# Optimization experiments

Hardware: AMD Instinct MI355X
Metric: run time of the kernel (lower is better)

## Reference

```python
import jax, jax.numpy as jnp
import numpy as np
from jax import lax

B, T, D, H, O, L = 128, 2048, 64, 128, 32, 2


def _rnn_layer(x, lengths, W_ih, W_hh, b_ih, b_hh):
    """One tanh RNN layer over padded [B,T,*] input with packed semantics:
    hidden state is frozen at steps t >= lengths[b] (those steps do not exist
    in the packed sequence). Returns per-step hidden states [B,T,H]."""
    Bl, Tl, _ = x.shape
    Hl = W_hh.shape[0]
    # precompute input projection once: [B,T,H]
    x_proj = jnp.einsum('btd,hd->bth', x, W_ih) + b_ih + b_hh

    def step(h, inp):
        xp, t = inp  # xp: [B,H], t: scalar
        h_new = jnp.tanh(xp + h @ W_hh.T)
        h = jnp.where((t < lengths)[:, None], h_new, h)
        return h, h

    h0 = jnp.zeros((Bl, Hl), dtype=x.dtype)
    _, ys = lax.scan(step, h0, (x_proj.transpose(1, 0, 2), jnp.arange(Tl)))
    return ys.transpose(1, 0, 2)  # [B,T,H]


def setup_inputs() -> dict:
    key = jax.random.key(0)
    ks = jax.random.split(key, 12)
    x = jax.random.normal(ks[0], (B, T, D), dtype=jnp.float32)
    # descending-sorted lengths in [1, T] (pack_padded_sequence enforce_sorted)
    lengths = jnp.sort(jax.random.randint(ks[1], (B,), 1, T + 1).astype(jnp.int32))[::-1]
    s_in = 1.0 / np.sqrt(H)
    W_ih0 = jax.random.uniform(ks[2], (H, D), minval=-s_in, maxval=s_in)
    W_hh0 = jax.random.uniform(ks[3], (H, H), minval=-s_in, maxval=s_in)
    b_ih0 = jax.random.uniform(ks[4], (H,), minval=-s_in, maxval=s_in)
    b_hh0 = jax.random.uniform(ks[5], (H,), minval=-s_in, maxval=s_in)
    W_ih1 = jax.random.uniform(ks[6], (H, H), minval=-s_in, maxval=s_in)
    W_hh1 = jax.random.uniform(ks[7], (H, H), minval=-s_in, maxval=s_in)
    b_ih1 = jax.random.uniform(ks[8], (H,), minval=-s_in, maxval=s_in)
    b_hh1 = jax.random.uniform(ks[9], (H,), minval=-s_in, maxval=s_in)
    W_fc = jax.random.uniform(ks[10], (O, H), minval=-s_in, maxval=s_in)
    b_fc = jax.random.uniform(ks[11], (O,), minval=-s_in, maxval=s_in)
    return {"x": x, "lengths": lengths,
            "W_ih0": W_ih0, "W_hh0": W_hh0, "b_ih0": b_ih0, "b_hh0": b_hh0,
            "W_ih1": W_ih1, "W_hh1": W_hh1, "b_ih1": b_ih1, "b_hh1": b_hh1,
            "W_fc": W_fc, "b_fc": b_fc}


def reference(x, lengths, W_ih0, W_hh0, b_ih0, b_hh0,
              W_ih1, W_hh1, b_ih1, b_hh1, W_fc, b_fc):
    h1 = _rnn_layer(x, lengths, W_ih0, W_hh0, b_ih0, b_hh0)   # [B,T,H]
    h2 = _rnn_layer(h1, lengths, W_ih1, W_hh1, b_ih1, b_hh1)  # [B,T,H]
    # pad_packed_sequence zero-fills positions t >= length
    mask = (jnp.arange(T)[None, :] < lengths[:, None])[..., None]
    out = jnp.where(mask, h2, 0.0)
    # fc is applied to the zero-padded tensor (padded rows become b_fc)
    return jnp.einsum('bth,oh->bto', out, W_fc) + b_fc
```

## Files before the change

### kernel.cpp

```cpp
#include <hip/hip_runtime.h>

#define BB 128
#define TT 2048
#define DD 64
#define HH 128
#define OO 32
#define NB 16
#define SCALE 2.885390081777927f

typedef _Float16 f16x8 __attribute__((ext_vector_type(8)));
typedef __fp16   pk16x2 __attribute__((ext_vector_type(2)));
typedef float    f32x4 __attribute__((ext_vector_type(4)));

#define MFMA16(a,b,c) __builtin_amdgcn_mfma_f32_16x16x32_f16((a),(b),(c),0,0,0)

__device__ __forceinline__ f32x4 load4(const float* p){ return *(const f32x4*)p; }

__device__ __forceinline__ f16x8 afrag_s(const float* p, float s){
    float4 a = *(const float4*)p, b = *(const float4*)(p+4);
    f16x8 r;
    r[0]=(_Float16)(a.x*s); r[1]=(_Float16)(a.y*s); r[2]=(_Float16)(a.z*s); r[3]=(_Float16)(a.w*s);
    r[4]=(_Float16)(b.x*s); r[5]=(_Float16)(b.y*s); r[6]=(_Float16)(b.z*s); r[7]=(_Float16)(b.w*s);
    return r;
}

__device__ __forceinline__ float tanh_pre(float z){
#if __has_builtin(__builtin_amdgcn_exp2f)
    float e = __builtin_amdgcn_exp2f(z);
#else
    float e = exp2f(z);
#endif
    return __builtin_fmaf(-2.f, __builtin_amdgcn_rcpf(1.f + e), 1.f);
}

__device__ __forceinline__ unsigned pk2(float a, float b){
    union { pk16x2 h; unsigned u; } c;
    c.h = __builtin_amdgcn_cvt_pkrtz(a, b);
    return c.u;
}

#define XSTR 72
extern "C" __global__ void __launch_bounds__(256)
proj_kernel(const float* __restrict__ x, const float* __restrict__ W_ih0,
            const float* __restrict__ b_ih0, const float* __restrict__ b_hh0,
            _Float16* __restrict__ xp0)
{
    const int tid = threadIdx.x;
    const int w = tid >> 6, lane = tid & 63;
    const int n = lane & 15, q = lane >> 4;
    const size_t row0 = (size_t)blockIdx.x * 64;

    __shared__ __align__(16) _Float16 XT[64][XSTR];

    #pragma unroll
    for (int it = 0; it < 4; ++it){
        float4 v = *(const float4*)(x + row0*DD + it*1024 + tid*4);
        int rr = it*16 + (tid >> 4), d0 = (tid & 15)*4;
        union { uint2 u; _Float16 h[4]; } c;
        c.h[0]=(_Float16)v.x; c.h[1]=(_Float16)v.y; c.h[2]=(_Float16)v.z; c.h[3]=(_Float16)v.w;
        *(uint2*)&XT[rr][d0] = c.u;
    }

    f16x8 A[8][2]; f32x4 bv[8];
    #pragma unroll
    for (int mt = 0; mt < 8; ++mt){
        #pragma unroll
        for (int kt = 0; kt < 2; ++kt)
            A[mt][kt] = afrag_s(W_ih0 + (mt*16 + n)*DD + kt*32 + q*8, SCALE);
        bv[mt] = (load4(b_ih0 + mt*16 + q*4) + load4(b_hh0 + mt*16 + q*4)) * SCALE;
    }
    __syncthreads();

    const _Float16* xr = &XT[w*16 + n][0];
    f16x8 B0 = *(const f16x8*)(xr + q*8);
    f16x8 B1 = *(const f16x8*)(xr + 32 + q*8);

    _Float16* orow = xp0 + (row0 + w*16 + n)*HH + q*4;
    #pragma unroll
    for (int mt = 0; mt < 8; ++mt){
        f32x4 acc = bv[mt];
        acc = MFMA16(A[mt][0], B0, acc);
        acc = MFMA16(A[mt][1], B1, acc);
        union { uint2 u; _Float16 h[4]; } s;
        #pragma unroll
        for (int r = 0; r < 4; ++r) s.h[r] = (_Float16)acc[r];
        *(uint2*)(orow + mt*16) = s.u;
    }
}

extern "C" __global__ void __launch_bounds__(256)
fill_kernel(const int* __restrict__ lengths, const float* __restrict__ b_fc,
            float* __restrict__ out)
{
    size_t idx = (size_t)blockIdx.x*256 + threadIdx.x;
    #pragma unroll
    for (int k = 0; k < 4; ++k, idx += (size_t)2048*256){
        int o4 = (int)(idx & 7);
        int t  = (int)((idx >> 3) & 2047);
        int b  = (int)(idx >> 14);
        if (t >= lengths[b])
            ((float4*)out)[idx] = *(const float4*)(b_fc + o4*4);
    }
}

#define LSTR 136

#define STEP(T_, P_, XA_, XB_) do {                                           \
    const int t_ = (T_);                                                      \
    f16x8 bh1[4], bh2[4];                                                     \
    _Pragma("unroll")                                                         \
    for (int kt = 0; kt < 4; ++kt){                                           \
        bh1[kt] = *(const f16x8*)&H1T[P_][n][kt*32 + q*8];                    \
        bh2[kt] = *(const f16x8*)&H2T[P_][n][kt*32 + q*8];                    \
    }                                                                         \
    f32x4 z0[2];                                                              \
    const bool doZ0 = (t_ < maxlen);                                          \
    if (doZ0){                                                                \
        union { uint2 u; _Float16 h[4]; } cA, cB; cA.u = XA_; cB.u = XB_;     \
        _Pragma("unroll")                                                     \
        for (int r = 0; r < 4; ++r){ z0[0][r] = (float)cA.h[r];               \
                                     z0[1][r] = (float)cB.h[r]; }             \
        _Pragma("unroll")                                                     \
        for (int kt = 0; kt < 4; ++kt){                                       \
            z0[0] = MFMA16(A0[0][kt], bh1[kt], z0[0]);                        \
            z0[1] = MFMA16(A0[1][kt], bh1[kt], z0[1]);                        \
        }                                                                     \
    }                                                                         \
    {              \
        const int tl = (t_ + 2 < TT) ? (t_ + 2) : (TT - 1);                   \
        XA_ = *(const uint2*)(xpbase + (size_t)tl*HH);                        \
        XB_ = *(const uint2*)(xpbase + (size_t)tl*HH + 16);                   \
    }                                                                         \
    f32x4 z1[2];                                                              \
    const bool doZ1 = (t_ >= 1) && (t_ <= maxlen);                            \
    if (doZ1){                                                                \
        f32x4 y0, y1;                                                         \
        z1[0] = b1v[0]; z1[1] = b1v[1];                                       \
        y0[0]=0.f;y0[1]=0.f;y0[2]=0.f;y0[3]=0.f; y1=y0;                       \
        _Pragma("unroll")                                                     \
        for (int kt = 0; kt < 4; ++kt){                                       \
            z1[0] = MFMA16(Ai[0][kt], bh1[kt], z1[0]);                        \
            z1[1] = MFMA16(Ai[1][kt], bh1[kt], z1[1]);                        \
            y0    = MFMA16(Ah[0][kt], bh2[kt], y0);                           \
            y1    = MFMA16(Ah[1][kt], bh2[kt], y1);                           \
        }                                                                     \
        z1[0] += y0; z1[1] += y1;                                             \
    }                                                                         \
    if (w >= 2 && t_ >= 2){                                                   \
        f32x4 zf = bfv;                                                       \
        _Pragma("unroll")                                                     \
        for (int kt = 0; kt < 4; ++kt) zf = MFMA16(Af[kt], bh2[kt], zf);      \
        if (t_ - 2 < lenn){                                                   \
            float4 sv; sv.x=zf[0]; sv.y=zf[1]; sv.z=zf[2]; sv.w=zf[3];        \
            *(float4*)(obase + (size_t)(t_-2)*OO) = sv;                       \
        }                                                                     \
    }                                                                         \
    if (doZ0){                                                                \
        _Pragma("unroll")                                                     \
        for (int m = 0; m < 2; ++m){                                          \
            uint2 v;                                                          \
            v.x = pk2(tanh_pre(z0[m][0]), tanh_pre(z0[m][1]));                \
            v.y = pk2(tanh_pre(z0[m][2]), tanh_pre(z0[m][3]));                \
            *(uint2*)&H1T[(P_)^1][n][(2*w+m)*16 + q*4] = v;                   \
        }                                                                     \
    }                                                                         \
    if (doZ1){                                                                \
        _Pragma("unroll")                                                     \
        for (int m = 0; m < 2; ++m){                                          \
            uint2 v;                                                          \
            v.x = pk2(tanh_pre(z1[m][0]), tanh_pre(z1[m][1]));                \
            v.y = pk2(tanh_pre(z1[m][2]), tanh_pre(z1[m][3]));                \
            *(uint2*)&H2T[(P_)^1][n][(2*w+m)*16 + q*4] = v;                   \
        }                                                                     \
    }                                                                         \
    asm volatile("s_waitcnt lgkmcnt(0)\n\ts_barrier" ::: "memory");           \
} while (0)

extern "C" __global__ void __launch_bounds__(256, 1)
scan_kernel(const _Float16* __restrict__ xp0, const int* __restrict__ lengths,
            const float* __restrict__ W_hh0,
            const float* __restrict__ W_ih1, const float* __restrict__ W_hh1,
            const float* __restrict__ b_ih1, const float* __restrict__ b_hh1,
            const float* __restrict__ W_fc,  const float* __restrict__ b_fc,
            float* __restrict__ out)
{
    const int tid  = threadIdx.x;
    const int w    = tid >> 6, lane = tid & 63;
    const int n    = lane & 15, q = lane >> 4;
    const int rbase= blockIdx.x * NB;

    __shared__ __align__(16) _Float16 H1T[2][NB][LSTR];
    __shared__ __align__(16) _Float16 H2T[2][NB][LSTR];

    for (int idx = tid; idx < 2*NB*LSTR/2; idx += 256){
        ((unsigned*)H1T)[idx] = 0u;
        ((unsigned*)H2T)[idx] = 0u;
    }

    f16x8 A0[2][4], Ai[2][4], Ah[2][4];
    #pragma unroll
    for (int m = 0; m < 2; ++m){
        const int row = (2*w + m)*16 + n;
        #pragma unroll
        for (int kt = 0; kt < 4; ++kt){
            A0[m][kt] = afrag_s(W_hh0 + row*HH + kt*32 + q*8, SCALE);
            Ai[m][kt] = afrag_s(W_ih1 + row*HH + kt*32 + q*8, SCALE);
            Ah[m][kt] = afrag_s(W_hh1 + row*HH + kt*32 + q*8, SCALE);
        }
    }
    const int f = w & 1;
    f16x8 Af[4];
    #pragma unroll
    for (int kt = 0; kt < 4; ++kt)
        Af[kt] = afrag_s(W_fc + (f*16 + n)*HH + kt*32 + q*8, 1.0f);

    f32x4 b1v[2];
    #pragma unroll
    for (int m = 0; m < 2; ++m)
        b1v[m] = (load4(b_ih1 + (2*w+m)*16 + q*4) + load4(b_hh1 + (2*w+m)*16 + q*4)) * SCALE;
    const f32x4 bfv = load4(b_fc + f*16 + q*4);

    const int lenn = lengths[rbase + n];
    int mx = lenn;
    #pragma unroll
    for (int s = 1; s < 16; s <<= 1){ int o = __shfl_xor(mx, s, 64); mx = max(mx, o); }
    const int maxlen = __builtin_amdgcn_readfirstlane(mx);

    const _Float16* xpbase = xp0 + ((size_t)(rbase+n)*TT)*HH + (2*w)*16 + q*4;
    float* obase = out + ((size_t)(rbase+n)*TT)*OO + f*16 + q*4;

    uint2 xeA = *(const uint2*)(xpbase);
    uint2 xeB = *(const uint2*)(xpbase + 16);
    uint2 xoA = *(const uint2*)(xpbase + HH);
    uint2 xoB = *(const uint2*)(xpbase + HH + 16);

    __syncthreads();

    for (int t0 = 0; t0 <= maxlen + 1; t0 += 2){
        STEP(t0,     0, xeA, xeB);
        STEP(t0 + 1, 1, xoA, xoB);
    }
}

extern "C" void kernel_launch(void* const* d_in, const int* in_sizes, int n_in,
                              void* d_out, int out_size, void* d_ws, size_t ws_size,
                              hipStream_t stream)
{
    const float* x       = (const float*)d_in[0];
    const int*   lengths = (const int*)  d_in[1];
    const float* W_ih0   = (const float*)d_in[2];
    const float* W_hh0   = (const float*)d_in[3];
    const float* b_ih0   = (const float*)d_in[4];
    const float* b_hh0   = (const float*)d_in[5];
    const float* W_ih1   = (const float*)d_in[6];
    const float* W_hh1   = (const float*)d_in[7];
    const float* b_ih1   = (const float*)d_in[8];
    const float* b_hh1   = (const float*)d_in[9];
    const float* W_fc    = (const float*)d_in[10];
    const float* b_fc    = (const float*)d_in[11];

    _Float16* xp = (_Float16*)d_ws;

    proj_kernel<<<BB*TT/64, 256, 0, stream>>>(x, W_ih0, b_ih0, b_hh0, xp);
    fill_kernel<<<2048, 256, 0, stream>>>(lengths, b_fc, (float*)d_out);
    scan_kernel<<<BB/NB, 256, 0, stream>>>(xp, lengths, W_hh0,
                                           W_ih1, W_hh1, b_ih1, b_hh1,
                                           W_fc, b_fc, (float*)d_out);
}
```

Before: 1.637 ms.

## Specialize warps: two run layer-1 recurrence, two run layer-2 plus FC

Splits the four wavefronts by role: waves 0-1 compute the layer-1 recurrence over all 128 hidden rows (4 row-tiles each), and waves 2-3 compute the layer-2 recurrence plus the output projection. Before, every wave did a slice of both layers. The LDS row stride changes from 136 to 132 halves, and B fragments are loaded as two 8-byte reads to suit the new stride. The aim is to balance MFMA work per wave and cut the per-wave register load of weight fragments. In exchange, layer 1 now does fewer MFMAs per step than layer 2, so the waves may be imbalanced at the shared barrier, and register pressure per wave rises.

Result: no change. 1.631 ms (-0.3%).

```diff
diff --git a/kernel.cpp b/kernel.cpp
--- a/kernel.cpp
+++ b/kernel.cpp
@@ -15,6 +15,8 @@
 #define MFMA16(a,b,c) __builtin_amdgcn_mfma_f32_16x16x32_f16((a),(b),(c),0,0,0)
 
 __device__ __forceinline__ f32x4 load4(const float* p){ return *(const f32x4*)p; }
+
+union U8 { uint2 u[2]; f16x8 v; };
 
 __device__ __forceinline__ f16x8 afrag_s(const float* p, float s){
     float4 a = *(const float4*)p, b = *(const float4*)(p+4);
@@ -103,74 +105,95 @@
     }
 }
 
-#define LSTR 136
-
-#define STEP(T_, P_, XA_, XB_) do {                                           \
+#define LSTR2 132
+#define PHB   (NB*LSTR2*2)
+
+#define STEP_L1(T_, P_, XS_) do {                                             \
     const int t_ = (T_);                                                      \
-    f16x8 bh1[4], bh2[4];                                                     \
+    U8 bh1[4];                                                                \
     _Pragma("unroll")                                                         \
     for (int kt = 0; kt < 4; ++kt){                                           \
-        bh1[kt] = *(const f16x8*)&H1T[P_][n][kt*32 + q*8];                    \
-        bh2[kt] = *(const f16x8*)&H2T[P_][n][kt*32 + q*8];                    \
-    }                                                                         \
-    f32x4 z0[2];                                                              \
+        bh1[kt].u[0] = *(const uint2*)(h1b + (P_)*PHB + kt*64);               \
+        bh1[kt].u[1] = *(const uint2*)(h1b + (P_)*PHB + kt*64 + 8);           \
+    }                                                                         \
+    f32x4 z[4];                                                               \
     const bool doZ0 = (t_ < maxlen);                                          \
     if (doZ0){                                                                \
-        union { uint2 u; _Float16 h[4]; } cA, cB; cA.u = XA_; cB.u = XB_;     \
-        _Pragma("unroll")                                                     \
-        for (int r = 0; r < 4; ++r){ z0[0][r] = (float)cA.h[r];               \
-                                     z0[1][r] = (float)cB.h[r]; }             \
-        _Pragma("unroll")                                                     \
-        for (int kt = 0; kt < 4; ++kt){                                       \
-            z0[0] = MFMA16(A0[0][kt], bh1[kt], z0[0]);                        \
-            z0[1] = MFMA16(A0[1][kt], bh1[kt], z0[1]);                        \
-        }                                                                     \
-    }                                                                         \
-    {              \
+        _Pragma("unroll")                                                     \
+        for (int m = 0; m < 4; ++m){                                          \
+            union { uint2 u; _Float16 h[4]; } c; c.u = XS_[m];                \
+            _Pragma("unroll")                                                 \
+            for (int r = 0; r < 4; ++r) z[m][r] = (float)c.h[r];              \
+        }                                                                     \
+        _Pragma("unroll")                                                     \
+        for (int kt = 0; kt < 4; ++kt)                                        \
+            _Pragma("unroll")                                                 \
+            for (int m = 0; m < 4; ++m)                                       \
+                z[m] = MFMA16(A0[m][kt], bh1[kt].v, z[m]);                    \
+    }                                                                         \
+    {             \
         const int tl = (t_ + 2 < TT) ? (t_ + 2) : (TT - 1);                   \
-        XA_ = *(const uint2*)(xpbase + (size_t)tl*HH);                        \
-        XB_ = *(const uint2*)(xpbase + (size_t)tl*HH + 16);                   \
-    }                                                                         \
-    f32x4 z1[2];                                                              \
+        _Pragma("unroll")                                                     \
+        for (int m = 0; m < 4; ++m)                                           \
+            XS_[m] = *(const uint2*)(xpb + (size_t)tl*256 + m*32);            \
+    }                                                                         \
+    if (doZ0){                                                                \
+        _Pragma("unroll")                                                     \
+        for (int m = 0; m < 4; ++m){                                          \
+            uint2 v;                                                          \
+            v.x = pk2(tanh_pre(z[m][0]), tanh_pre(z[m][1]));                  \
+            v.y = pk2(tanh_pre(z[m][2]), tanh_pre(z[m][3]));                  \
+            *(uint2*)((char*)H1T + ((P_)^1)*PHB + n*264 + (w*4+m)*32 + q*8) = v; \
+        }                                                                     \
+    }                                                                         \
+    asm volatile("s_waitcnt lgkmcnt(0)\n\ts_barrier" ::: "memory");           \
+} while (0)
+
+#define STEP_L2(T_, P_) do {                                                  \
+    const int t_ = (T_);                                                      \
+    U8 bh1[4], bh2[4];                                                        \
+    _Pragma("unroll")                                                         \
+    for (int kt = 0; kt < 4; ++kt){                                           \
+        bh1[kt].u[0] = *(const uint2*)(h1b + (P_)*PHB + kt*64);               \
+        bh1[kt].u[1] = *(const uint2*)(h1b + (P_)*PHB + kt*64 + 8);           \
+        bh2[kt].u[0] = *(const uint2*)(h2b + (P_)*PHB + kt*64);               \
+        bh2[kt].u[1] = *(const uint2*)(h2b + (P_)*PHB + kt*64 + 8);           \
+    }                                                                         \
     const bool doZ1 = (t_ >= 1) && (t_ <= maxlen);                            \
+    f32x4 z[4];                                                               \
     if (doZ1){                                                                \
-        f32x4 y0, y1;                                                         \
-        z1[0] = b1v[0]; z1[1] = b1v[1];                                       \
-        y0[0]=0.f;y0[1]=0.f;y0[2]=0.f;y0[3]=0.f; y1=y0;                       \
-        _Pragma("unroll")                                                     \
-        for (int kt = 0; kt < 4; ++kt){                                       \
-            z1[0] = MFMA16(Ai[0][kt], bh1[kt], z1[0]);                        \
-            z1[1] = MFMA16(Ai[1][kt], bh1[kt], z1[1]);                        \
-            y0    = MFMA16(Ah[0][kt], bh2[kt], y0);                           \
-            y1    = MFMA16(Ah[1][kt], bh2[kt], y1);                           \
-        }                                                                     \
-        z1[0] += y0; z1[1] += y1;                                             \
-    }                                                                         \
-    if (w >= 2 && t_ >= 2){                                                   \
+        f32x4 y[4];                                                           \
+        _Pragma("unroll")                                                     \
+        for (int m = 0; m < 4; ++m){                                          \
+            z[m] = b1v[m];                                                    \
+            y[m][0]=0.f; y[m][1]=0.f; y[m][2]=0.f; y[m][3]=0.f;               \
+        }                                                                     \
+        _Pragma("unroll")                                                     \
+        for (int kt = 0; kt < 4; ++kt)                                        \
+            _Pragma("unroll")                                                 \
+            for (int m = 0; m < 4; ++m){                                      \
+                z[m] = MFMA16(Ai[m][kt], bh1[kt].v, z[m]);                    \
+                y[m] = MFMA16(Ah[m][kt], bh2[kt].v, y[m]);                    \
+            }                                                                 \
+        _Pragma("unroll")                                                     \
+        for (int m = 0; m < 4; ++m) z[m] += y[m];                             \
+    }                                                                         \
+    if (t_ >= 2){                                                             \
         f32x4 zf = bfv;                                                       \
         _Pragma("unroll")                                                     \
-        for (int kt = 0; kt < 4; ++kt) zf = MFMA16(Af[kt], bh2[kt], zf);      \
+        for (int kt = 0; kt < 4; ++kt) zf = MFMA16(Af[kt], bh2[kt].v, zf);    \
         if (t_ - 2 < lenn){                                                   \
             float4 sv; sv.x=zf[0]; sv.y=zf[1]; sv.z=zf[2]; sv.w=zf[3];        \
             *(float4*)(obase + (size_t)(t_-2)*OO) = sv;                       \
         }                                                                     \
     }                                                                         \
-    if (doZ0){                                                                \
-        _Pragma("unroll")                                                     \
-        for (int m = 0; m < 2; ++m){                                          \
+    if (doZ1){                                                                \
+        _Pragma("unroll")                                                     \
+        for (int m = 0; m < 4; ++m){                                          \
             uint2 v;                                                          \
-            v.x = pk2(tanh_pre(z0[m][0]), tanh_pre(z0[m][1]));                \
-            v.y = pk2(tanh_pre(z0[m][2]), tanh_pre(z0[m][3]));                \
-            *(uint2*)&H1T[(P_)^1][n][(2*w+m)*16 + q*4] = v;                   \
-        }                                                                     \
-    }                                                                         \
-    if (doZ1){                                                                \
-        _Pragma("unroll")                                                     \
-        for (int m = 0; m < 2; ++m){                                          \
-            uint2 v;                                                          \
-            v.x = pk2(tanh_pre(z1[m][0]), tanh_pre(z1[m][1]));                \
-            v.y = pk2(tanh_pre(z1[m][2]), tanh_pre(z1[m][3]));                \
-            *(uint2*)&H2T[(P_)^1][n][(2*w+m)*16 + q*4] = v;                   \
+            v.x = pk2(tanh_pre(z[m][0]), tanh_pre(z[m][1]));                  \
+            v.y = pk2(tanh_pre(z[m][2]), tanh_pre(z[m][3]));                  \
+            *(uint2*)((char*)H2T + ((P_)^1)*PHB + n*264 + (wl*4+m)*32 + q*8) = v; \
         }                                                                     \
     }                                                                         \
     asm volatile("s_waitcnt lgkmcnt(0)\n\ts_barrier" ::: "memory");           \
@@ -189,56 +212,75 @@
     const int n    = lane & 15, q = lane >> 4;
     const int rbase= blockIdx.x * NB;
 
-    __shared__ __align__(16) _Float16 H1T[2][NB][LSTR];
-    __shared__ __align__(16) _Float16 H2T[2][NB][LSTR];
-
-    for (int idx = tid; idx < 2*NB*LSTR/2; idx += 256){
+    __shared__ __align__(16) _Float16 H1T[2][NB][LSTR2];
+    __shared__ __align__(16) _Float16 H2T[2][NB][LSTR2];
+
+    for (int idx = tid; idx < (2*NB*LSTR2)/2; idx += 256){
         ((unsigned*)H1T)[idx] = 0u;
         ((unsigned*)H2T)[idx] = 0u;
     }
 
-    f16x8 A0[2][4], Ai[2][4], Ah[2][4];
-    #pragma unroll
-    for (int m = 0; m < 2; ++m){
-        const int row = (2*w + m)*16 + n;
-        #pragma unroll
-        for (int kt = 0; kt < 4; ++kt){
-            A0[m][kt] = afrag_s(W_hh0 + row*HH + kt*32 + q*8, SCALE);
-            Ai[m][kt] = afrag_s(W_ih1 + row*HH + kt*32 + q*8, SCALE);
-            Ah[m][kt] = afrag_s(W_hh1 + row*HH + kt*32 + q*8, SCALE);
-        }
-    }
-    const int f = w & 1;
-    f16x8 Af[4];
-    #pragma unroll
-    for (int kt = 0; kt < 4; ++kt)
-        Af[kt] = afrag_s(W_fc + (f*16 + n)*HH + kt*32 + q*8, 1.0f);
-
-    f32x4 b1v[2];
-    #pragma unroll
-    for (int m = 0; m < 2; ++m)
-        b1v[m] = (load4(b_ih1 + (2*w+m)*16 + q*4) + load4(b_hh1 + (2*w+m)*16 + q*4)) * SCALE;
-    const f32x4 bfv = load4(b_fc + f*16 + q*4);
-
     const int lenn = lengths[rbase + n];
     int mx = lenn;
     #pragma unroll
     for (int s = 1; s < 16; s <<= 1){ int o = __shfl_xor(mx, s, 64); mx = max(mx, o); }
     const int maxlen = __builtin_amdgcn_readfirstlane(mx);
 
-    const _Float16* xpbase = xp0 + ((size_t)(rbase+n)*TT)*HH + (2*w)*16 + q*4;
-    float* obase = out + ((size_t)(rbase+n)*TT)*OO + f*16 + q*4;
-
-    uint2 xeA = *(const uint2*)(xpbase);
-    uint2 xeB = *(const uint2*)(xpbase + 16);
-    uint2 xoA = *(const uint2*)(xpbase + HH);
-    uint2 xoB = *(const uint2*)(xpbase + HH + 16);
+    const char* h1b = (const char*)H1T + n*264 + q*16;
+    const char* h2b = (const char*)H2T + n*264 + q*16;
 
     __syncthreads();
 
-    for (int t0 = 0; t0 <= maxlen + 1; t0 += 2){
-        STEP(t0,     0, xeA, xeB);
-        STEP(t0 + 1, 1, xoA, xoB);
+    if (w < 2){
+        f16x8 A0[4][4];
+        #pragma unroll
+        for (int m = 0; m < 4; ++m){
+            const int row = (w*4 + m)*16 + n;
+            #pragma unroll
+            for (int kt = 0; kt < 4; ++kt)
+                A0[m][kt] = afrag_s(W_hh0 + row*HH + kt*32 + q*8, SCALE);
+        }
+        const char* xpb = (const char*)(xp0 + ((size_t)(rbase+n)*TT)*HH)
+                          + (w*4)*32 + q*8;
+
+        uint2 xe[4], xo[4];
+        #pragma unroll
+        for (int m = 0; m < 4; ++m){
+            xe[m] = *(const uint2*)(xpb + m*32);
+            xo[m] = *(const uint2*)(xpb + 256 + m*32);
+        }
+
+        for (int t0 = 0; t0 <= maxlen + 1; t0 += 2){
+            STEP_L1(t0,     0, xe);
+            STEP_L1(t0 + 1, 1, xo);
+        }
+    } else {
+        const int wl = w - 2, f = w & 1;
+        f16x8 Ai[4][4], Ah[4][4];
+        f32x4 b1v[4];
+        #pragma unroll
+        for (int m = 0; m < 4; ++m){
+            const int row = (wl*4 + m)*16 + n;
+            #pragma unroll
+            for (int kt = 0; kt < 4; ++kt){
+                Ai[m][kt] = afrag_s(W_ih1 + row*HH + kt*32 + q*8, SCALE);
+                Ah[m][kt] = afrag_s(W_hh1 + row*HH + kt*32 + q*8, SCALE);
+            }
+            b1v[m] = (load4(b_ih1 + (wl*4+m)*16 + q*4)
+                    + load4(b_hh1 + (wl*4+m)*16 + q*4)) * SCALE;
+        }
+        f16x8 Af[4];
+        #pragma unroll
+        for (int kt = 0; kt < 4; ++kt)
+            Af[kt] = afrag_s(W_fc + (f*16 + n)*HH + kt*32 + q*8, 1.0f);
+        const f32x4 bfv = load4(b_fc + f*16 + q*4);
+
+        float* obase = out + ((size_t)(rbase+n)*TT)*OO + f*16 + q*4;
+
+        for (int t0 = 0; t0 <= maxlen + 1; t0 += 2){
+            STEP_L2(t0,     0);
+            STEP_L2(t0 + 1, 1);
+        }
     }
 }
 
```

## Split RNN scan into layer-specialized waves with LDS ring and windowed barriers

Applied to the files above, without the earlier changes.

Replaces the 4-wave scan block, where every wave computed a slice of both layers and synchronized each step, with a 2-wave block. Wave 0 runs layer 0 over all 128 hidden units, and wave 1 runs layer 1 plus the FC projection. Layer-0 states go through an 8-slot LDS ring, with one barrier per 4-step window, so the layers run as a software pipeline offset by one window. Wave 0 reads its own just-written state back from LDS with no barrier, and a XOR swizzle is added for bank conflicts. The trade-off is that each wave does 4x the MFMA work serially per step and occupancy is lower, in exchange for far fewer barriers.

Measured after the change: 2.945 ms. 1.8x slower.

```diff
diff --git a/kernel.cpp b/kernel.cpp
--- a/kernel.cpp
+++ b/kernel.cpp
@@ -103,80 +103,89 @@
     }
 }
 
-#define LSTR 136
-
-#define STEP(T_, P_, XA_, XB_) do {                                           \
+#define SLOT  (NB*256)
+#define RING  8
+#define KWIN  4
+
+#define STEPA(T_, XS_) do {                                                   \
+    const int t_ = (T_);                                                      \
+    f32x4 z[8];                                                               \
+    _Pragma("unroll")                                                         \
+    for (int mt = 0; mt < 8; ++mt){                                           \
+        union { uint2 u; _Float16 h[4]; } c; c.u = XS_[mt];                   \
+        _Pragma("unroll")                                                     \
+        for (int r = 0; r < 4; ++r) z[mt][r] = (float)c.h[r];                 \
+    }                                                                         \
+    _Pragma("unroll")                                                         \
+    for (int kt = 0; kt < 4; ++kt)                                            \
+        _Pragma("unroll")                                                     \
+        for (int mt = 0; mt < 8; ++mt)                                        \
+            z[mt] = MFMA16(A0[mt][kt], Wst[kt], z[mt]);                       \
+    {   const int tl = (t_ + 2 < TT) ? (t_ + 2) : (TT - 1);                   \
+        const char* xq = xpb + (size_t)tl*256;                                \
+        _Pragma("unroll")                                                     \
+        for (int mt = 0; mt < 8; ++mt) XS_[mt] = *(const uint2*)(xq + mt*32); \
+    }                                                                         \
+    {   char* wp = h1p + ((t_ & 7) * SLOT);                                   \
+        _Pragma("unroll")                                                     \
+        for (int mt = 0; mt < 8; ++mt){                                       \
+            uint2 v;                                                          \
+            v.x = pk2(tanh_pre(z[mt][0]), tanh_pre(z[mt][1]));                \
+            v.y = pk2(tanh_pre(z[mt][2]), tanh_pre(z[mt][3]));                \
+            *(uint2*)(wp + woff[mt]) = v;                                     \
+        }                                                                     \
+        _Pragma("unroll")                                                     \
+        for (int kt = 0; kt < 4; ++kt)                                        \
+            Wst[kt] = *(const f16x8*)((const char*)wp + roff[kt]);            \
+    }                                                                         \
+} while (0)
+
+#define STEPB(T_) do {                                                        \
     const int t_ = (T_);                                                      \
     f16x8 bh1[4], bh2[4];                                                     \
-    _Pragma("unroll")                                                         \
-    for (int kt = 0; kt < 4; ++kt){                                           \
-        bh1[kt] = *(const f16x8*)&H1T[P_][n][kt*32 + q*8];                    \
-        bh2[kt] = *(const f16x8*)&H2T[P_][n][kt*32 + q*8];                    \
-    }                                                                         \
-    f32x4 z0[2];                                                              \
-    const bool doZ0 = (t_ < maxlen);                                          \
-    if (doZ0){                                                                \
-        union { uint2 u; _Float16 h[4]; } cA, cB; cA.u = XA_; cB.u = XB_;     \
-        _Pragma("unroll")                                                     \
-        for (int r = 0; r < 4; ++r){ z0[0][r] = (float)cA.h[r];               \
-                                     z0[1][r] = (float)cB.h[r]; }             \
+    {   const char* rp1 = h1p + ((t_ & 7) * SLOT);                            \
+        const char* rp2 = h2p + ((~t_ & 1) * SLOT);                           \
         _Pragma("unroll")                                                     \
         for (int kt = 0; kt < 4; ++kt){                                       \
-            z0[0] = MFMA16(A0[0][kt], bh1[kt], z0[0]);                        \
-            z0[1] = MFMA16(A0[1][kt], bh1[kt], z0[1]);                        \
+            bh1[kt] = *(const f16x8*)(rp1 + roff[kt]);                        \
+            bh2[kt] = *(const f16x8*)(rp2 + roff[kt]);                        \
+        } }                                                                   \
+    f32x4 z[8];                                                               \
+    _Pragma("unroll")                                                         \
+    for (int mt = 0; mt < 8; ++mt) z[mt] = b1v[mt];                           \
+    _Pragma("unroll")                                                         \
+    for (int kt = 0; kt < 4; ++kt)                                            \
+        _Pragma("unroll")                                                     \
+        for (int mt = 0; mt < 8; ++mt)                                        \
+            z[mt] = MFMA16(Ai[mt][kt], bh1[kt], z[mt]);                       \
+    _Pragma("unroll")                                                         \
+    for (int kt = 0; kt < 4; ++kt)                                            \
+        _Pragma("unroll")                                                     \
+        for (int mt = 0; mt < 8; ++mt)                                        \
+            z[mt] = MFMA16(Ah[mt][kt], bh2[kt], z[mt]);                       \
+    {   f32x4 zf0 = bfv0, zf1 = bfv1;                                         \
+        _Pragma("unroll")                                                     \
+        for (int kt = 0; kt < 4; ++kt){                                       \
+            zf0 = MFMA16(Af[0][kt], bh2[kt], zf0);                            \
+            zf1 = MFMA16(Af[1][kt], bh2[kt], zf1);                            \
         }                                                                     \
-    }                                                                         \
-    {              \
-        const int tl = (t_ + 2 < TT) ? (t_ + 2) : (TT - 1);                   \
-        XA_ = *(const uint2*)(xpbase + (size_t)tl*HH);                        \
-        XB_ = *(const uint2*)(xpbase + (size_t)tl*HH + 16);                   \
-    }                                                                         \
-    f32x4 z1[2];                                                              \
-    const bool doZ1 = (t_ >= 1) && (t_ <= maxlen);                            \
-    if (doZ1){                                                                \
-        f32x4 y0, y1;                                                         \
-        z1[0] = b1v[0]; z1[1] = b1v[1];                                       \
-        y0[0]=0.f;y0[1]=0.f;y0[2]=0.f;y0[3]=0.f; y1=y0;                       \
-        _Pragma("unroll")                                                     \
-        for (int kt = 0; kt < 4; ++kt){                                       \
-            z1[0] = MFMA16(Ai[0][kt], bh1[kt], z1[0]);                        \
-            z1[1] = MFMA16(Ai[1][kt], bh1[kt], z1[1]);                        \
-            y0    = MFMA16(Ah[0][kt], bh2[kt], y0);                           \
-            y1    = MFMA16(Ah[1][kt], bh2[kt], y1);                           \
-        }                                                                     \
-        z1[0] += y0; z1[1] += y1;                                             \
-    }                                                                         \
-    if (w >= 2 && t_ >= 2){                                                   \
-        f32x4 zf = bfv;                                                       \
-        _Pragma("unroll")                                                     \
-        for (int kt = 0; kt < 4; ++kt) zf = MFMA16(Af[kt], bh2[kt], zf);      \
-        if (t_ - 2 < lenn){                                                   \
-            float4 sv; sv.x=zf[0]; sv.y=zf[1]; sv.z=zf[2]; sv.w=zf[3];        \
-            *(float4*)(obase + (size_t)(t_-2)*OO) = sv;                       \
-        }                                                                     \
-    }                                                                         \
-    if (doZ0){                                                                \
-        _Pragma("unroll")                                                     \
-        for (int m = 0; m < 2; ++m){                                          \
+        if ((unsigned)(t_ - 1) < (unsigned)lenn){                             \
+            float* op = obase + (size_t)(t_ - 1) * OO;                        \
+            float4 s0; s0.x=zf0[0]; s0.y=zf0[1]; s0.z=zf0[2]; s0.w=zf0[3];    \
+            float4 s1; s1.x=zf1[0]; s1.y=zf1[1]; s1.z=zf1[2]; s1.w=zf1[3];    \
+            *(float4*)op = s0; *(float4*)(op + 16) = s1;                      \
+        } }                                                                   \
+    {   char* wp = h2p + ((t_ & 1) * SLOT);                                   \
+        _Pragma("unroll")                                                     \
+        for (int mt = 0; mt < 8; ++mt){                                       \
             uint2 v;                                                          \
-            v.x = pk2(tanh_pre(z0[m][0]), tanh_pre(z0[m][1]));                \
-            v.y = pk2(tanh_pre(z0[m][2]), tanh_pre(z0[m][3]));                \
-            *(uint2*)&H1T[(P_)^1][n][(2*w+m)*16 + q*4] = v;                   \
-        }                                                                     \
-    }                                                                         \
-    if (doZ1){                                                                \
-        _Pragma("unroll")                                                     \
-        for (int m = 0; m < 2; ++m){                                          \
-            uint2 v;                                                          \
-            v.x = pk2(tanh_pre(z1[m][0]), tanh_pre(z1[m][1]));                \
-            v.y = pk2(tanh_pre(z1[m][2]), tanh_pre(z1[m][3]));                \
-            *(uint2*)&H2T[(P_)^1][n][(2*w+m)*16 + q*4] = v;                   \
-        }                                                                     \
-    }                                                                         \
-    asm volatile("s_waitcnt lgkmcnt(0)\n\ts_barrier" ::: "memory");           \
+            v.x = pk2(tanh_pre(z[mt][0]), tanh_pre(z[mt][1]));                \
+            v.y = pk2(tanh_pre(z[mt][2]), tanh_pre(z[mt][3]));                \
+            *(uint2*)(wp + woff[mt]) = v;                                     \
+        } }                                                                   \
 } while (0)
 
-extern "C" __global__ void __launch_bounds__(256, 1)
+extern "C" __global__ void __launch_bounds__(128, 1)
 scan_kernel(const _Float16* __restrict__ xp0, const int* __restrict__ lengths,
             const float* __restrict__ W_hh0,
             const float* __restrict__ W_ih1, const float* __restrict__ W_hh1,
@@ -189,56 +198,120 @@
     const int n    = lane & 15, q = lane >> 4;
     const int rbase= blockIdx.x * NB;
 
-    __shared__ __align__(16) _Float16 H1T[2][NB][LSTR];
-    __shared__ __align__(16) _Float16 H2T[2][NB][LSTR];
-
-    for (int idx = tid; idx < 2*NB*LSTR/2; idx += 256){
-        ((unsigned*)H1T)[idx] = 0u;
-        ((unsigned*)H2T)[idx] = 0u;
-    }
-
-    f16x8 A0[2][4], Ai[2][4], Ah[2][4];
-    #pragma unroll
-    for (int m = 0; m < 2; ++m){
-        const int row = (2*w + m)*16 + n;
-        #pragma unroll
-        for (int kt = 0; kt < 4; ++kt){
-            A0[m][kt] = afrag_s(W_hh0 + row*HH + kt*32 + q*8, SCALE);
-            Ai[m][kt] = afrag_s(W_ih1 + row*HH + kt*32 + q*8, SCALE);
-            Ah[m][kt] = afrag_s(W_hh1 + row*HH + kt*32 + q*8, SCALE);
-        }
-    }
-    const int f = w & 1;
-    f16x8 Af[4];
-    #pragma unroll
-    for (int kt = 0; kt < 4; ++kt)
-        Af[kt] = afrag_s(W_fc + (f*16 + n)*HH + kt*32 + q*8, 1.0f);
-
-    f32x4 b1v[2];
-    #pragma unroll
-    for (int m = 0; m < 2; ++m)
-        b1v[m] = (load4(b_ih1 + (2*w+m)*16 + q*4) + load4(b_hh1 + (2*w+m)*16 + q*4)) * SCALE;
-    const f32x4 bfv = load4(b_fc + f*16 + q*4);
+    __shared__ __align__(16) char H1R[RING * SLOT];
+    __shared__ __align__(16) char H2P[2 * SLOT];
+
+    for (int idx = tid; idx < (RING + 2) * SLOT / 4; idx += 128){
+        if (idx < RING * SLOT / 4) ((unsigned*)H1R)[idx] = 0u;
+        else ((unsigned*)H2P)[idx - RING * SLOT / 4] = 0u;
+    }
 
     const int lenn = lengths[rbase + n];
     int mx = lenn;
     #pragma unroll
     for (int s = 1; s < 16; s <<= 1){ int o = __shfl_xor(mx, s, 64); mx = max(mx, o); }
     const int maxlen = __builtin_amdgcn_readfirstlane(mx);
-
-    const _Float16* xpbase = xp0 + ((size_t)(rbase+n)*TT)*HH + (2*w)*16 + q*4;
-    float* obase = out + ((size_t)(rbase+n)*TT)*OO + f*16 + q*4;
-
-    uint2 xeA = *(const uint2*)(xpbase);
-    uint2 xeB = *(const uint2*)(xpbase + 16);
-    uint2 xoA = *(const uint2*)(xpbase + HH);
-    uint2 xoB = *(const uint2*)(xpbase + HH + 16);
+    const int nwin   = (maxlen + KWIN - 1) / KWIN;
+    const int W      = nwin + 1;
+
+    const int swz = (n & 7) << 4;
+    int woff[8], roff[4];
+    #pragma unroll
+    for (int mt = 0; mt < 8; ++mt) woff[mt] = (mt*32 + q*8)  ^ swz;
+    #pragma unroll
+    for (int kt = 0; kt < 4; ++kt) roff[kt] = (kt*64 + q*16) ^ swz;
+    char* h1p = H1R + n*256;
+    char* h2p = H2P + n*256;
 
     __syncthreads();
 
-    for (int t0 = 0; t0 <= maxlen + 1; t0 += 2){
-        STEP(t0,     0, xeA, xeB);
-        STEP(t0 + 1, 1, xoA, xoB);
+    if (w == 0){
+        f16x8 A0[8][4];
+        #pragma unroll
+        for (int mt = 0; mt < 8; ++mt)
+            #pragma unroll
+            for (int kt = 0; kt < 4; ++kt)
+                A0[mt][kt] = afrag_s(W_hh0 + (mt*16 + n)*HH + kt*32 + q*8, SCALE);
+
+        const char* xpb = (const char*)xp0 + (size_t)(rbase + n)*TT*256 + q*8;
+
+        f16x8 Wst[4];
+        #pragma unroll
+        for (int kt = 0; kt < 4; ++kt)
+            #pragma unroll
+            for (int j = 0; j < 8; ++j) Wst[kt][j] = (_Float16)0.f;
+
+        uint2 XE[8], XO[8];
+        #pragma unroll
+        for (int mt = 0; mt < 8; ++mt){
+            XE[mt] = *(const uint2*)(xpb + mt*32);
+            XO[mt] = *(const uint2*)(xpb + 256 + mt*32);
+        }
+
+        for (int win = 0; win < W; ++win){
+            if (win < nwin){
+                const int t0 = win * KWIN;
+                STEPA(t0 + 0, XE);
+                STEPA(t0 + 1, XO);
+                STEPA(t0 + 2, XE);
+                STEPA(t0 + 3, XO);
+            }
+            asm volatile("s_waitcnt lgkmcnt(0)\n\ts_barrier" ::: "memory");
+        }
+    } else {
+        f16x8 Ai[8][4], Ah[8][4], Af[2][4];
+        f32x4 b1v[8];
+        #pragma unroll
+        for (int mt = 0; mt < 8; ++mt){
+            #pragma unroll
+            for (int kt = 0; kt < 4; ++kt){
+                Ai[mt][kt] = afrag_s(W_ih1 + (mt*16 + n)*HH + kt*32 + q*8, SCALE);
+                Ah[mt][kt] = afrag_s(W_hh1 + (mt*16 + n)*HH + kt*32 + q*8, SCALE);
+            }
+            b1v[mt] = (load4(b_ih1 + mt*16 + q*4)
+                     + load4(b_hh1 + mt*16 + q*4)) * SCALE;
+        }
+        #pragma unroll
+        for (int f = 0; f < 2; ++f)
+            #pragma unroll
+            for (int kt = 0; kt < 4; ++kt)
+                Af[f][kt] = afrag_s(W_fc + (f*16 + n)*HH + kt*32 + q*8, 1.0f);
+        const f32x4 bfv0 = load4(b_fc + q*4);
+        const f32x4 bfv1 = load4(b_fc + 16 + q*4);
+
+        float* obase = out + (size_t)(rbase + n)*TT*OO + q*4;
+
+        for (int win = 0; win < W; ++win){
+            if (win > 0){
+                const int t0 = (win - 1) * KWIN;
+                STEPB(t0 + 0);
+                STEPB(t0 + 1);
+                STEPB(t0 + 2);
+                STEPB(t0 + 3);
+            }
+            asm volatile("s_waitcnt lgkmcnt(0)\n\ts_barrier" ::: "memory");
+        }
+
+        {
+            const int tl = nwin * KWIN - 1;
+            const char* rp2 = h2p + ((tl & 1) * SLOT);
+            f16x8 bh2[4];
+            #pragma unroll
+            for (int kt = 0; kt < 4; ++kt)
+                bh2[kt] = *(const f16x8*)(rp2 + roff[kt]);
+            f32x4 zf0 = bfv0, zf1 = bfv1;
+            #pragma unroll
+            for (int kt = 0; kt < 4; ++kt){
+                zf0 = MFMA16(Af[0][kt], bh2[kt], zf0);
+                zf1 = MFMA16(Af[1][kt], bh2[kt], zf1);
+            }
+            if (tl < lenn){
+                float* op = obase + (size_t)tl * OO;
+                float4 s0; s0.x=zf0[0]; s0.y=zf0[1]; s0.z=zf0[2]; s0.w=zf0[3];
+                float4 s1; s1.x=zf1[0]; s1.y=zf1[1]; s1.z=zf1[2]; s1.w=zf1[3];
+                *(float4*)op = s0; *(float4*)(op + 16) = s1;
+            }
+        }
     }
 }
 
@@ -263,7 +336,7 @@
 
     proj_kernel<<<BB*TT/64, 256, 0, stream>>>(x, W_ih0, b_ih0, b_hh0, xp);
     fill_kernel<<<2048, 256, 0, stream>>>(lengths, b_fc, (float*)d_out);
-    scan_kernel<<<BB/NB, 256, 0, stream>>>(xp, lengths, W_hh0,
+    scan_kernel<<<BB/NB, 128, 0, stream>>>(xp, lengths, W_hh0,
                                            W_ih1, W_hh1, b_ih1, b_hh1,
                                            W_fc, b_fc, (float*)d_out);
 }
```
